# Kernel tuning notes

Measured on AMD Instinct MI355X. Metric: run time of the kernel, lower is better.

The kernel has to match this reference:

```python
import jax, jax.numpy as jnp
import numpy as np

N_EMBD = 1024
N_HEAD = 16


def setup_inputs() -> dict:
    key = jax.random.key(0)
    ks = jax.random.split(key, 5)
    C = N_EMBD
    x = jax.random.normal(ks[0], (4, 2048, C), dtype=jnp.float32)
    # linear params, scaled like torch default init (~U(-1/sqrt(C),1/sqrt(C)))
    s = 1.0 / np.sqrt(C)
    W_attn = jax.random.uniform(ks[1], (C, 3 * C), jnp.float32, -s, s)
    b_attn = jax.random.uniform(ks[2], (3 * C,), jnp.float32, -s, s)
    W_proj = jax.random.uniform(ks[3], (C, C), jnp.float32, -s, s)
    b_proj = jax.random.uniform(ks[4], (C,), jnp.float32, -s, s)
    return {"x": x, "W_attn": W_attn, "b_attn": b_attn, "W_proj": W_proj, "b_proj": b_proj}


def reference(x, W_attn, b_attn, W_proj, b_proj):
    B, T, C = x.shape
    H = N_HEAD
    D = C // H
    qkv = x @ W_attn + b_attn                      # [B,T,3C]
    q, k, v = jnp.split(qkv, 3, axis=-1)
    # [B,T,C] -> [B,H,T,D]
    q = q.reshape(B, T, H, D).transpose(0, 2, 1, 3)
    k = k.reshape(B, T, H, D).transpose(0, 2, 1, 3)
    v = v.reshape(B, T, H, D).transpose(0, 2, 1, 3)
    scale = 1.0 / np.sqrt(D).astype(np.float32)
    att = jnp.einsum('bhqd,bhkd->bhqk', q, k) * scale  # [B,H,T,T]
    causal = jnp.tril(jnp.ones((T, T), dtype=bool))
    att = jnp.where(causal[None, None], att, -jnp.inf)
    att = jax.nn.softmax(att, axis=-1)
    y = jnp.einsum('bhqk,bhkd->bhqd', att, v)      # [B,H,T,D]
    y = y.transpose(0, 2, 1, 3).reshape(B, T, C)
    return y @ W_proj + b_proj
```

## Files before the change

kernel.cpp:

```cpp
#include <hip/hip_runtime.h>
#include <hip/hip_bf16.h>
#include <math.h>


typedef __bf16 bf16x8 __attribute__((ext_vector_type(8)));
typedef float f32x4 __attribute__((ext_vector_type(4)));
typedef float f32x16 __attribute__((ext_vector_type(16)));

__device__ __forceinline__ f32x4 mfma16(bf16x8 a, bf16x8 b, f32x4 c) {
    return __builtin_amdgcn_mfma_f32_16x16x32_bf16(a, b, c, 0, 0, 0);
}
__device__ __forceinline__ f32x16 mfma32(bf16x8 a, bf16x8 b, f32x16 c) {
    return __builtin_amdgcn_mfma_f32_32x32x16_bf16(a, b, c, 0, 0, 0);
}

#define GLOBAL_AS __attribute__((address_space(1)))
#define LDS_AS __attribute__((address_space(3)))

__device__ __forceinline__ void async_copy16(const __hip_bfloat16* g, __hip_bfloat16* l) {
    __builtin_amdgcn_global_load_lds((const GLOBAL_AS uint32_t*)g, (LDS_AS uint32_t*)l, 16, 0, 0);
}

__device__ __forceinline__ uint32_t cvtpk(float lo, float hi) {
    uint32_t r;
    asm("v_cvt_pk_bf16_f32 %0, %1, %2" : "=v"(r) : "v"(lo), "v"(hi));
    return r;
}

#define QSCL 0.18033688011112042f

__global__ __launch_bounds__(256) void cast_x_kernel(const float* __restrict__ in,
                                                     __hip_bfloat16* __restrict__ out, int n) {
    int i = (blockIdx.x * 256 + threadIdx.x) * 8;
    if (i >= n) return;
    union { __hip_bfloat16 h[8]; uint4 v; } tmp;
#pragma unroll
    for (int j = 0; j < 8; ++j) tmp.h[j] = __float2bfloat16(in[i + j]);
    *reinterpret_cast<uint4*>(out + i) = tmp.v;
}

__global__ __launch_bounds__(256) void transpose_cast_kernel(const float* __restrict__ in,
                                                             __hip_bfloat16* __restrict__ out,
                                                             int R, int Cc) {
    __shared__ float tile[32][33];
    int c0 = blockIdx.x * 32, r0 = blockIdx.y * 32;
    int tx = threadIdx.x & 31, ty = threadIdx.x >> 5;
#pragma unroll
    for (int i = 0; i < 4; ++i) {
        int r = r0 + ty + i * 8;
        tile[ty + i * 8][tx] = in[(size_t)r * Cc + c0 + tx];
    }
    __syncthreads();
#pragma unroll
    for (int i = 0; i < 4; ++i) {
        int c = c0 + ty + i * 8;
        out[(size_t)c * R + r0 + tx] = __float2bfloat16(tile[tx][ty + i * 8]);
    }
}

#define GEMM128_BODY(A_, Bt_, K_)                                                       \
    __shared__ __hip_bfloat16 As[128 * 32];                                             \
    __shared__ __hip_bfloat16 Bs[128 * 32];                                             \
    const int tid = threadIdx.x;                                                        \
    const int w = tid >> 6;                                                             \
    const int lr = tid & 15, lh = (tid & 63) >> 4;                                      \
    const int wr = w >> 1, wc = w & 1;                                                  \
    f32x4 zero = {0.f, 0.f, 0.f, 0.f};                                                  \
    f32x4 acc[4][4];                                                                    \
    _Pragma("unroll") for (int i = 0; i < 4; ++i)                                       \
        _Pragma("unroll") for (int j = 0; j < 4; ++j) acc[i][j] = zero;                 \
    for (int k0 = 0; k0 < (K_); k0 += 32) {                                             \
        _Pragma("unroll") for (int i = 0; i < 2; ++i) {                                 \
            int t = i * 256 + tid;                                                      \
            async_copy16((A_) + (size_t)(m0 + (t >> 2)) * (K_) + k0 + (t & 3) * 8,      \
                         As + (size_t)(i * 256 + w * 64) * 8);                          \
            async_copy16((Bt_) + (size_t)(n0 + (t >> 2)) * (K_) + k0 + (t & 3) * 8,     \
                         Bs + (size_t)(i * 256 + w * 64) * 8);                          \
        }                                                                               \
        __syncthreads();                                                                \
        bf16x8 af[4], bf[4];                                                            \
        _Pragma("unroll") for (int mf = 0; mf < 4; ++mf)                                \
            af[mf] = *reinterpret_cast<const bf16x8*>(                                  \
                &As[(wr * 64 + mf * 16 + lr) * 32 + lh * 8]);                           \
        _Pragma("unroll") for (int nf = 0; nf < 4; ++nf)                                \
            bf[nf] = *reinterpret_cast<const bf16x8*>(                                  \
                &Bs[(wc * 64 + nf * 16 + lr) * 32 + lh * 8]);                           \
        _Pragma("unroll") for (int mf = 0; mf < 4; ++mf)                                \
            _Pragma("unroll") for (int nf = 0; nf < 4; ++nf)                            \
                acc[mf][nf] = mfma16(af[mf], bf[nf], acc[mf][nf]);                      \
        __syncthreads();                                                                \
    }

__global__ __launch_bounds__(256) void gemm_qkv_kernel(
    const __hip_bfloat16* __restrict__ A, const __hip_bfloat16* __restrict__ Bt,
    const float* __restrict__ bias,
    __hip_bfloat16* __restrict__ qd, __hip_bfloat16* __restrict__ kd,
    __hip_bfloat16* __restrict__ vtd) {
    const int K = 1024;
    const int m0 = blockIdx.x * 128;
    const int n0 = blockIdx.y * 128;
    GEMM128_BODY(A, Bt, K)

    const int region = n0 >> 10;
#pragma unroll
    for (int mf = 0; mf < 4; ++mf) {
#pragma unroll
        for (int nf = 0; nf < 4; ++nf) {
            int n = n0 + wc * 64 + nf * 16 + lr;
            float bv = bias[n];
            int mbase = m0 + wr * 64 + mf * 16 + 4 * lh;
            int bb = mbase >> 11;
            int t = mbase & 2047;
            int c = n & 1023, hh = c >> 6, dd = c & 63;
            if (region == 2) {
                union { __hip_bfloat16 h[4]; uint2 v; } pk;
#pragma unroll
                for (int r = 0; r < 4; ++r) pk.h[r] = __float2bfloat16(acc[mf][nf][r] + bv);
                *reinterpret_cast<uint2*>(
                    &vtd[(((size_t)bb * 16 + hh) * 64 + dd) * 2048 + t]) = pk.v;
            } else if (region == 0) {
#pragma unroll
                for (int r = 0; r < 4; ++r)
                    qd[(((size_t)bb * 16 + hh) * 2048 + t + r) * 64 + dd] =
                        __float2bfloat16((acc[mf][nf][r] + bv) * QSCL);
            } else {
#pragma unroll
                for (int r = 0; r < 4; ++r)
                    kd[(((size_t)bb * 16 + hh) * 2048 + t + r) * 64 + dd] =
                        __float2bfloat16(acc[mf][nf][r] + bv);
            }
        }
    }
}

__global__ __launch_bounds__(256) void gemm_proj_kernel(
    const __hip_bfloat16* __restrict__ A, const __hip_bfloat16* __restrict__ Bt,
    const float* __restrict__ bias, float* __restrict__ out) {
    const int K = 1024, N = 1024;
    const int m0 = blockIdx.x * 128;
    const int n0 = blockIdx.y * 128;
    GEMM128_BODY(A, Bt, K)

#pragma unroll
    for (int nf = 0; nf < 4; ++nf) {
        int n = n0 + wc * 64 + nf * 16 + lr;
        float bv = bias[n];
#pragma unroll
        for (int mf = 0; mf < 4; ++mf) {
            int mbase = m0 + wr * 64 + mf * 16 + 4 * lh;
#pragma unroll
            for (int r = 0; r < 4; ++r)
                out[(size_t)(mbase + r) * N + n] = acc[mf][nf][r] + bv;
        }
    }
}

__global__ __launch_bounds__(512) void attn_kernel(
    const __hip_bfloat16* __restrict__ q, const __hip_bfloat16* __restrict__ k,
    const __hip_bfloat16* __restrict__ vt, __hip_bfloat16* __restrict__ y) {
    const int T = 2048, D = 64, C = 1024;
    const float THR = 8.0f;

    int wid = ((int)blockIdx.x & 7) * 64 + ((int)blockIdx.x >> 3);
    int bh = wid >> 3;
    int qr = wid & 7;
    int q256 = (wid & 32) ? qr : 7 - qr;
    int b = bh >> 4, h = bh & 15;
    int tid = threadIdx.x;
    int w = tid >> 6, l = tid & 63;
    int ql = l & 31, hi = l >> 5;

    __shared__ __hip_bfloat16 Ks[64 * 64];
    __shared__ __hip_bfloat16 Vs[64 * 64];
    __shared__ __hip_bfloat16 Pt[8][32][36];

    const int q0 = q256 * 256 + w * 32;
    const __hip_bfloat16* kbh = k + (size_t)bh * T * D;
    const __hip_bfloat16* vbh = vt + (size_t)bh * D * T;

    bf16x8 qf[4];
#pragma unroll
    for (int c = 0; c < 4; ++c)
        qf[c] = *reinterpret_cast<const bf16x8*>(
            q + ((size_t)bh * T + q0 + ql) * D + c * 16 + hi * 8);

    f32x16 o0 = {}, o1 = {};
    float m = -INFINITY, lp = 0.f;

    const int lastSub = q0 >> 5;
    const int nt64 = 4 * q256 + 4;

    for (int t64 = 0; t64 < nt64; ++t64) {
        __syncthreads();
        {
            int slot = tid;
            int row = slot >> 3;
            int fold = ((row & 7) ^ (row >> 3)) & 7;
            int colb = ((slot & 7) * 16) ^ (fold << 4);
            async_copy16(kbh + (size_t)(t64 * 64 + row) * 64 + (colb >> 1),
                         Ks + (size_t)(w * 64) * 8);
            async_copy16(vbh + (size_t)row * T + t64 * 64 + (colb >> 1),
                         Vs + (size_t)(w * 64) * 8);
        }
        __syncthreads();

#pragma unroll
        for (int sub = 0; sub < 2; ++sub) {
            const int is = t64 * 2 + sub;
            if (is > lastSub) break;
            bf16x8 kf[4];
            {
                int krow = sub * 32 + ql;
                int kfold = ((krow & 7) ^ (krow >> 3)) & 7;
                const char* KsB = reinterpret_cast<const char*>(Ks) + krow * 128;
#pragma unroll
                for (int c = 0; c < 4; ++c)
                    kf[c] = *reinterpret_cast<const bf16x8*>(
                        KsB + ((c * 32 + hi * 16) ^ (kfold << 4)));
            }

            __builtin_amdgcn_s_setprio(1);
            f32x16 s = {};
            s = mfma32(kf[0], qf[0], s);
            s = mfma32(kf[1], qf[1], s);
            s = mfma32(kf[2], qf[2], s);
            s = mfma32(kf[3], qf[3], s);
            __builtin_amdgcn_s_setprio(0);

            bf16x8 vf[2][2];
#pragma unroll
            for (int dblk = 0; dblk < 2; ++dblk) {
                int vrow = dblk * 32 + ql;
                int vfold = ((vrow & 7) ^ (vrow >> 3)) & 7;
                const char* VsB = reinterpret_cast<const char*>(Vs) + vrow * 128;
#pragma unroll
                for (int sl = 0; sl < 2; ++sl)
                    vf[dblk][sl] = *reinterpret_cast<const bf16x8*>(
                        VsB + ((sub * 64 + sl * 32 + hi * 16) ^ (vfold << 4)));
            }

            if (is == lastSub) {
#pragma unroll
                for (int r = 0; r < 16; ++r) {
                    int kvrow = (r & 3) + 8 * (r >> 2) + 4 * hi;
                    if (kvrow > ql) s[r] = -INFINITY;
                }
            }

            float mx;
            {
                float a = fmaxf(fmaxf(s[0], s[1]), s[2]);
                float bq = fmaxf(fmaxf(s[3], s[4]), s[5]);
                float c = fmaxf(fmaxf(s[6], s[7]), s[8]);
                float d = fmaxf(fmaxf(s[9], s[10]), s[11]);
                float e = fmaxf(fmaxf(s[12], s[13]), s[14]);
                mx = fmaxf(fmaxf(fmaxf(a, bq), fmaxf(c, d)), fmaxf(e, s[15]));
            }
            mx = fmaxf(mx, __shfl_xor(mx, 32));

            if (!__all(mx - m <= THR)) {
                float mnew = fmaxf(m, mx);
                float al = __builtin_amdgcn_exp2f(m - mnew);
                m = mnew;
                lp *= al;
#pragma unroll
                for (int r = 0; r < 16; ++r) { o0[r] *= al; o1[r] *= al; }
            }

#pragma unroll
            for (int r = 0; r < 16; ++r) s[r] = __builtin_amdgcn_exp2f(s[r] - m);

            lp += ((s[0] + s[1]) + (s[2] + s[3])) + ((s[4] + s[5]) + (s[6] + s[7])) +
                  (((s[8] + s[9]) + (s[10] + s[11])) + ((s[12] + s[13]) + (s[14] + s[15])));

            {
                uint2 w0, w1, w2, w3;
                w0.x = cvtpk(s[0], s[1]);   w0.y = cvtpk(s[2], s[3]);
                w1.x = cvtpk(s[4], s[5]);   w1.y = cvtpk(s[6], s[7]);
                w2.x = cvtpk(s[8], s[9]);   w2.y = cvtpk(s[10], s[11]);
                w3.x = cvtpk(s[12], s[13]); w3.y = cvtpk(s[14], s[15]);
                *reinterpret_cast<uint2*>(&Pt[w][ql][4 * hi])      = w0;
                *reinterpret_cast<uint2*>(&Pt[w][ql][8 + 4 * hi])  = w1;
                *reinterpret_cast<uint2*>(&Pt[w][ql][16 + 4 * hi]) = w2;
                *reinterpret_cast<uint2*>(&Pt[w][ql][24 + 4 * hi]) = w3;
            }

            union { uint32_t u[4]; bf16x8 v; } pa0, pa1;
            {
                uint2 r0 = *reinterpret_cast<const uint2*>(&Pt[w][ql][8 * hi]);
                uint2 r1 = *reinterpret_cast<const uint2*>(&Pt[w][ql][8 * hi + 4]);
                uint2 r2 = *reinterpret_cast<const uint2*>(&Pt[w][ql][16 + 8 * hi]);
                uint2 r3 = *reinterpret_cast<const uint2*>(&Pt[w][ql][16 + 8 * hi + 4]);
                pa0.u[0] = r0.x; pa0.u[1] = r0.y; pa0.u[2] = r1.x; pa0.u[3] = r1.y;
                pa1.u[0] = r2.x; pa1.u[1] = r2.y; pa1.u[2] = r3.x; pa1.u[3] = r3.y;
            }

            __builtin_amdgcn_s_setprio(1);
            o0 = mfma32(vf[0][0], pa0.v, o0);
            o0 = mfma32(vf[0][1], pa1.v, o0);
            o1 = mfma32(vf[1][0], pa0.v, o1);
            o1 = mfma32(vf[1][1], pa1.v, o1);
            __builtin_amdgcn_s_setprio(0);
        }
    }

    lp += __shfl_xor(lp, 32);
    float inv = 1.0f / lp;

    __hip_bfloat16* yq = y + ((size_t)b * T + q0 + ql) * C + h * 64;
#pragma unroll
    for (int dblk = 0; dblk < 2; ++dblk) {
#pragma unroll
        for (int g = 0; g < 4; ++g) {
            union { __hip_bfloat16 h4[4]; uint2 v; } pkk;
#pragma unroll
            for (int r = 0; r < 4; ++r) {
                float val = (dblk ? o1[g * 4 + r] : o0[g * 4 + r]) * inv;
                pkk.h4[r] = __float2bfloat16(val);
            }
            *reinterpret_cast<uint2*>(yq + dblk * 32 + g * 8 + hi * 4) = pkk.v;
        }
    }
}

extern "C" void kernel_launch(void* const* d_in, const int* in_sizes, int n_in,
                              void* d_out, int out_size, void* d_ws, size_t ws_size,
                              hipStream_t stream) {
    const float* x      = (const float*)d_in[0];
    const float* W_attn = (const float*)d_in[1];
    const float* b_attn = (const float*)d_in[2];
    const float* W_proj = (const float*)d_in[3];
    const float* b_proj = (const float*)d_in[4];
    float* out = (float*)d_out;

    __hip_bfloat16* wsb = reinterpret_cast<__hip_bfloat16*>(d_ws);
    __hip_bfloat16* xb  = wsb;
    __hip_bfloat16* WaT = xb + (size_t)8192 * 1024;
    __hip_bfloat16* WpT = WaT + (size_t)3072 * 1024;
    __hip_bfloat16* qd  = WpT + (size_t)1024 * 1024;
    __hip_bfloat16* kd  = qd + (size_t)64 * 2048 * 64;
    __hip_bfloat16* vtd = kd + (size_t)64 * 2048 * 64;
    __hip_bfloat16* ya  = vtd + (size_t)64 * 2048 * 64;

    cast_x_kernel<<<4096, 256, 0, stream>>>(x, xb, 8192 * 1024);
    transpose_cast_kernel<<<dim3(96, 32), 256, 0, stream>>>(W_attn, WaT, 1024, 3072);
    transpose_cast_kernel<<<dim3(32, 32), 256, 0, stream>>>(W_proj, WpT, 1024, 1024);
    gemm_qkv_kernel<<<dim3(64, 24), 256, 0, stream>>>(xb, WaT, b_attn, qd, kd, vtd);
    attn_kernel<<<512, 512, 0, stream>>>(qd, kd, vtd, ya);
    gemm_proj_kernel<<<dim3(64, 8), 256, 0, stream>>>(ya, WpT, b_proj, out);
}
```

Before: 172.6 us.

## Double-buffer GEMM LDS tiles with 64-wide K and prefetch two stages ahead

Rewrites the shared GEMM body to use two LDS buffers holding 64-wide K tiles. Async global-to-LDS loads for tile t+2 are issued while tile t+1 is computed, so memory latency overlaps with MFMA work. It also halves the number of barriers per K step. In exchange, LDS use quadruples, which may reduce occupancy. The 128-byte row stride may also cause more LDS bank conflicts on fragment reads.

```diff
diff --git a/kernel.cpp b/kernel.cpp
--- a/kernel.cpp
+++ b/kernel.cpp
@@ -58,37 +58,53 @@
     }
 }
 
-#define GEMM128_BODY(A_, Bt_, K_)                                                       \
-    __shared__ __hip_bfloat16 As[128 * 32];                                             \
-    __shared__ __hip_bfloat16 Bs[128 * 32];                                             \
-    const int tid = threadIdx.x;                                                        \
-    const int w = tid >> 6;                                                             \
-    const int lr = tid & 15, lh = (tid & 63) >> 4;                                      \
-    const int wr = w >> 1, wc = w & 1;                                                  \
-    f32x4 zero = {0.f, 0.f, 0.f, 0.f};                                                  \
-    f32x4 acc[4][4];                                                                    \
-    _Pragma("unroll") for (int i = 0; i < 4; ++i)                                       \
-        _Pragma("unroll") for (int j = 0; j < 4; ++j) acc[i][j] = zero;                 \
-    for (int k0 = 0; k0 < (K_); k0 += 32) {                                             \
-        _Pragma("unroll") for (int i = 0; i < 2; ++i) {                                 \
-            int t = i * 256 + tid;                                                      \
-            async_copy16((A_) + (size_t)(m0 + (t >> 2)) * (K_) + k0 + (t & 3) * 8,      \
-                         As + (size_t)(i * 256 + w * 64) * 8);                          \
-            async_copy16((Bt_) + (size_t)(n0 + (t >> 2)) * (K_) + k0 + (t & 3) * 8,     \
-                         Bs + (size_t)(i * 256 + w * 64) * 8);                          \
-        }                                                                               \
-        __syncthreads();                                                                \
-        bf16x8 af[4], bf[4];                                                            \
-        _Pragma("unroll") for (int mf = 0; mf < 4; ++mf)                                \
-            af[mf] = *reinterpret_cast<const bf16x8*>(                                  \
-                &As[(wr * 64 + mf * 16 + lr) * 32 + lh * 8]);                           \
-        _Pragma("unroll") for (int nf = 0; nf < 4; ++nf)                                \
-            bf[nf] = *reinterpret_cast<const bf16x8*>(                                  \
-                &Bs[(wc * 64 + nf * 16 + lr) * 32 + lh * 8]);                           \
-        _Pragma("unroll") for (int mf = 0; mf < 4; ++mf)                                \
-            _Pragma("unroll") for (int nf = 0; nf < 4; ++nf)                            \
-                acc[mf][nf] = mfma16(af[mf], bf[nf], acc[mf][nf]);                      \
-        __syncthreads();                                                                \
+#define GEMM128_BODY(A_, Bt_, K_)                                                      \
+    __shared__ __hip_bfloat16 As[2][128 * 64];                                         \
+    __shared__ __hip_bfloat16 Bs[2][128 * 64];                                         \
+    const int tid = threadIdx.x;                                                       \
+    const int w = tid >> 6;                                                            \
+    const int lr = tid & 15, lh = (tid & 63) >> 4;                                     \
+    const int wr = w >> 1, wc = w & 1;                                                 \
+    f32x4 zero = {0.f, 0.f, 0.f, 0.f};                                                 \
+    f32x4 acc[4][4];                                                                   \
+    _Pragma("unroll") for (int i = 0; i < 4; ++i)                                      \
+        _Pragma("unroll") for (int j = 0; j < 4; ++j) acc[i][j] = zero;                \
+    const int nt = (K_) >> 6;                                                          \
+    auto stage_ = [&](int d_, int t_) {                                                \
+        int kb = t_ * 64;                                                              \
+        _Pragma("unroll") for (int ld = 0; ld < 4; ++ld) {                             \
+            int s = ld * 256 + tid;                                                    \
+            int row = s >> 3, ke = (s & 7) * 8;                                        \
+            async_copy16((A_) + (size_t)(m0 + row) * (K_) + kb + ke,                   \
+                         &As[d_][(ld * 256 + w * 64) * 8]);                            \
+            async_copy16((Bt_) + (size_t)(n0 + row) * (K_) + kb + ke,                  \
+                         &Bs[d_][(ld * 256 + w * 64) * 8]);                            \
+        }                                                                              \
+    };                                                                                 \
+    stage_(0, 0);                                                                      \
+    stage_(1, 1);                                                                      \
+    asm volatile("s_waitcnt vmcnt(8)" ::: "memory");                                   \
+    __builtin_amdgcn_s_barrier();                                                      \
+    __builtin_amdgcn_sched_barrier(0);                                                 \
+    for (int t = 0; t < nt; ++t) {                                                     \
+        const int d = t & 1;                                                           \
+        bf16x8 bfr[4][2];                                                              \
+        _Pragma("unroll") for (int nf = 0; nf < 4; ++nf)                               \
+            _Pragma("unroll") for (int kk = 0; kk < 2; ++kk)                           \
+                bfr[nf][kk] = *reinterpret_cast<const bf16x8*>(                        \
+                    &Bs[d][(wc * 64 + nf * 16 + lr) * 64 + kk * 32 + lh * 8]);         \
+        _Pragma("unroll") for (int mf = 0; mf < 4; ++mf) {                             \
+            bf16x8 af0 = *reinterpret_cast<const bf16x8*>(                             \
+                &As[d][(wr * 64 + mf * 16 + lr) * 64 + lh * 8]);                       \
+            bf16x8 af1 = *reinterpret_cast<const bf16x8*>(                             \
+                &As[d][(wr * 64 + mf * 16 + lr) * 64 + 32 + lh * 8]);                  \
+            _Pragma("unroll") for (int nf = 0; nf < 4; ++nf) {                         \
+                acc[mf][nf] = mfma16(af0, bfr[nf][0], acc[mf][nf]);                    \
+                acc[mf][nf] = mfma16(af1, bfr[nf][1], acc[mf][nf]);                    \
+            }                                                                          \
+        }                                                                              \
+        if (t + 1 < nt) __syncthreads();                                               \
+        if (t + 2 < nt) stage_(d, t + 2);                                              \
     }
 
 __global__ __launch_bounds__(256) void gemm_qkv_kernel(
```

New measurement: 181.9 us. +5.4%, slower.
